# Kernel optimization log

Hardware: AMD Instinct MI355X
Metric: run time of the kernel (lower is better)

The kernel has to match this reference:

```python
import jax, jax.numpy as jnp
import numpy as np

EPS = 1e-7
C = 1.0  # Poincare ball curvature

def _norm(v):
    return jnp.maximum(jnp.linalg.norm(v, axis=-1, keepdims=True), EPS)

def logmap0(x):
    n = _norm(x)
    n_c = jnp.minimum(n, 1.0 - 1e-5)
    return jnp.arctanh(jnp.sqrt(C) * n_c) * x / (jnp.sqrt(C) * n)

def expmap0(v):
    n = _norm(v)
    return jnp.tanh(jnp.sqrt(C) * n) * v / (jnp.sqrt(C) * n)

def hat_layer(x, W, a_src, a_dst, src, dst, num_nodes):
    # x: [N, in] on manifold; W: [in, H*D]; a_src/a_dst: [H, D]
    H, D = a_src.shape
    h = logmap0(x) @ W                       # tangent-space linear, [N, H*D]
    h = h.reshape(num_nodes, H, D)
    e_s = jnp.einsum('nhd,hd->nh', h, a_src)  # [N, H]
    e_d = jnp.einsum('nhd,hd->nh', h, a_dst)
    e = jax.nn.leaky_relu(e_s[src] + e_d[dst], 0.2)          # [E, H]
    emax = jax.ops.segment_max(e, dst, num_segments=num_nodes)
    emax = jnp.where(jnp.isfinite(emax), emax, 0.0)
    ee = jnp.exp(e - emax[dst])                               # [E, H]
    denom = jax.ops.segment_sum(ee, dst, num_segments=num_nodes)
    alpha = ee / (denom[dst] + 1e-16)                          # segment softmax
    msg = alpha[:, :, None] * h[src]                           # [E, H, D] (largest buffer)
    out = jax.ops.segment_sum(msg, dst, num_segments=num_nodes)
    return expmap0(out.reshape(num_nodes, H * D))

def setup_inputs() -> dict:
    key = jax.random.key(0)
    ks = jax.random.split(key, 9)
    N, E = 50000, 800000
    IN, HID, OUT, HEADS = 128, 64, 64, 4
    x = 0.05 * jax.random.normal(ks[0], (N, IN), dtype=jnp.float32)  # inside unit ball
    edge_index0 = jax.random.randint(ks[1], (2, E), 0, N, dtype=jnp.int32)
    edge_index1 = jax.random.randint(ks[2], (2, E), 0, N, dtype=jnp.int32)
    s = 0.05
    W1 = s * jax.random.normal(ks[3], (IN, HEADS * HID), dtype=jnp.float32)
    a_src1 = s * jax.random.normal(ks[4], (HEADS, HID), dtype=jnp.float32)
    a_dst1 = s * jax.random.normal(ks[5], (HEADS, HID), dtype=jnp.float32)
    W2 = s * jax.random.normal(ks[6], (HEADS * HID, OUT), dtype=jnp.float32)
    a_src2 = s * jax.random.normal(ks[7], (1, OUT), dtype=jnp.float32)
    a_dst2 = s * jax.random.normal(ks[8], (1, OUT), dtype=jnp.float32)
    return {"x": x, "W1": W1, "a_src1": a_src1, "a_dst1": a_dst1,
            "W2": W2, "a_src2": a_src2, "a_dst2": a_dst2,
            "edge_index0": edge_index0, "edge_index1": edge_index1}

def reference(x, W1, a_src1, a_dst1, W2, a_src2, a_dst2, edge_index0, edge_index1):
    N = x.shape[0]
    h = hat_layer(x, W1, a_src1, a_dst1, edge_index0[0], edge_index0[1], N)
    out = hat_layer(h, W2, a_src2, a_dst2, edge_index1[0], edge_index1[1], N)
    return out
```

## Files before the change

kernel.cpp:

```cpp
#include <hip/hip_runtime.h>

#define EPSF 1e-7f
#define NBMAX 512

typedef __attribute__((ext_vector_type(4))) _Float16 half4;
typedef __attribute__((ext_vector_type(8))) _Float16 half8;
typedef __attribute__((ext_vector_type(2))) _Float16 half2v;
typedef __attribute__((ext_vector_type(4))) float f32x4;
typedef unsigned long long u64;

__device__ __forceinline__ float lrelu02(float x){ return x > 0.f ? x : 0.2f*x; }

__global__ __launch_bounds__(256) void k_pre(
    const float* __restrict__ W1, const float* __restrict__ W2,
    const float* __restrict__ x,
    _Float16* __restrict__ w1t, _Float16* __restrict__ w2t,
    int* __restrict__ bcnt, _Float16* __restrict__ lxh, int N) {
  const int b = blockIdx.x, tid = threadIdx.x;
  if (b < 128) {
    int idx = b*256 + tid;
    int j = idx >> 7, k = idx & 127;
    w1t[idx] = (_Float16)W1[(size_t)k*256 + j];
    return;
  }
  if (b < 192) {
    int idx = (b-128)*256 + tid;
    int j = idx >> 8, k = idx & 255;
    w2t[idx] = (_Float16)W2[(size_t)k*64 + j];
    return;
  }
  if (b == 192) {
    for (int i = tid; i < 2*NBMAX; i += 256) bcnt[i] = 0;
    return;
  }
  int tidg = (b - 193)*256 + tid;
  int wid = tidg >> 6, lane = tidg & 63;
  int nw = (gridDim.x - 193) * 4;
  for (int row = wid; row < N; row += nw) {
    float2 v = *(const float2*)(x + (size_t)row*128 + lane*2);
    float ss = v.x*v.x + v.y*v.y;
    #pragma unroll
    for (int o = 32; o; o >>= 1) ss += __shfl_xor(ss, o);
    float n  = fmaxf(sqrtf(ss), EPSF);
    float nc = fminf(n, 1.f - 1e-5f);
    float sc = atanhf(nc) / n;
    half2v hv; hv.x = (_Float16)(v.x*sc); hv.y = (_Float16)(v.y*sc);
    *(half2v*)(lxh + (size_t)row*128 + lane*2) = hv;
  }
}

__global__ __launch_bounds__(256) void k_bhist(
    const int* __restrict__ dst0, int E0, const int* __restrict__ dst1, int E1,
    int* __restrict__ bcnt0, int* __restrict__ bcnt1, int nb) {
  __shared__ int h0[NBMAX], h1[NBMAX];
  const int tid = threadIdx.x;
  const int g = blockIdx.x*blockDim.x + tid;
  const int stride = gridDim.x*blockDim.x;
  for (int i = tid; i < nb; i += 256) { h0[i] = 0; h1[i] = 0; }
  __syncthreads();
  for (int i = g; i < E0; i += stride) atomicAdd(&h0[dst0[i] >> 7], 1);
  for (int i = g; i < E1; i += stride) atomicAdd(&h1[dst1[i] >> 7], 1);
  __syncthreads();
  for (int i = tid; i < nb; i += 256) {
    if (h0[i]) atomicAdd(&bcnt0[i], h0[i]);
    if (h1[i]) atomicAdd(&bcnt1[i], h1[i]);
  }
}

__global__ __launch_bounds__(1024) void k_bscan(
    const int* __restrict__ bcnt0, int* __restrict__ bbase0, int* __restrict__ bcur0,
    const int* __restrict__ bcnt1, int* __restrict__ bbase1, int* __restrict__ bcur1,
    int nb) {
  __shared__ int wt[16];
  const int tid = threadIdx.x;
  const int half = tid >> 9, idx = tid & 511;
  const int* bcnt = half ? bcnt1 : bcnt0;
  int* bbase = half ? bbase1 : bbase0;
  int* bcur  = half ? bcur1  : bcur0;
  int v = (idx < nb) ? bcnt[idx] : 0;
  const int lane = tid & 63, w = tid >> 6;
  int inc = v;
  #pragma unroll
  for (int o = 1; o < 64; o <<= 1) { int t = __shfl_up(inc, o); if (lane >= o) inc += t; }
  if (lane == 63) wt[w] = inc;
  __syncthreads();
  int woff = 0;
  for (int i = half*8; i < w; ++i) woff += wt[i];
  int excl = woff + inc - v;
  if (idx < nb) { bbase[idx] = excl; bcur[idx] = excl; }
  if (idx == nb-1) bbase[nb] = excl + v;
}

__global__ __launch_bounds__(256) void k_bucketA(
    const int* __restrict__ src0, const int* __restrict__ dst0,
    int* __restrict__ bcur0, u64* __restrict__ temp0, int E0, int blocksA0,
    const int* __restrict__ src1, const int* __restrict__ dst1,
    int* __restrict__ bcur1, u64* __restrict__ temp1, int E1, int nb) {
  const int g0 = (blockIdx.x < blocksA0);
  const int* src = g0 ? src0 : src1;
  const int* dst = g0 ? dst0 : dst1;
  int* bcur      = g0 ? bcur0 : bcur1;
  u64* temp      = g0 ? temp0 : temp1;
  const int E    = g0 ? E0 : E1;
  const int cb   = g0 ? blockIdx.x : blockIdx.x - blocksA0;
  __shared__ int hist[NBMAX];
  __shared__ int lbase[NBMAX];
  const int tid = threadIdx.x;
  const int chunk0 = cb * 4096;
  const int e_end = min(chunk0 + 4096, E);
  for (int i = tid; i < nb; i += 256) hist[i] = 0;
  __syncthreads();
  for (int i = chunk0 + tid; i < e_end; i += 256)
    atomicAdd(&hist[dst[i] >> 7], 1);
  __syncthreads();
  for (int bn = tid; bn < nb; bn += 256) {
    int c = hist[bn];
    lbase[bn] = c ? atomicAdd(&bcur[bn], c) : 0;
    hist[bn] = 0;
  }
  __syncthreads();
  for (int i = chunk0 + tid; i < e_end; i += 256) {
    int d = dst[i];
    int bn = d >> 7;
    int off = atomicAdd(&hist[bn], 1);
    temp[(size_t)lbase[bn] + off] = ((u64)(unsigned)d << 32) | (unsigned)src[i];
  }
}

__global__ __launch_bounds__(256) void k_bucketB2(
    const u64* __restrict__ temp0, const int* __restrict__ bbase0,
    int* __restrict__ rowptr0, int* __restrict__ csrc0,
    const float* __restrict__ es1, const float* __restrict__ ed1,
    half4* __restrict__ w0,
    const u64* __restrict__ temp1, const int* __restrict__ bbase1,
    int* __restrict__ rowptr1, int* __restrict__ csrc1, int N, int nb) {
  const int g0 = (blockIdx.x < nb);
  const u64* temp = g0 ? temp0 : temp1;
  const int* bbase = g0 ? bbase0 : bbase1;
  int* rowptr = g0 ? rowptr0 : rowptr1;
  int* csrc   = g0 ? csrc0 : csrc1;
  const int b = g0 ? blockIdx.x : blockIdx.x - nb;
  __shared__ int lcnt[128];
  __shared__ int lcur[128];
  __shared__ int wt4[4];
  __shared__ float ledv[512];
  const int tid = threadIdx.x;
  const int d0 = b << 7;
  const int d1 = min(d0 + 128, N);
  const int lo = bbase[b], hi = bbase[b+1];
  if (tid < 128) lcnt[tid] = 0;
  if (g0) {
    for (int i = tid; i < (d1 - d0)*4; i += 256) ledv[i] = ed1[d0*4 + i];
  }
  __syncthreads();
  for (int k = lo + tid; k < hi; k += 256)
    atomicAdd(&lcnt[(int)(temp[k] >> 32) - d0], 1);
  __syncthreads();
  int v = (tid < 128) ? lcnt[tid] : 0;
  const int lane = tid & 63, w = tid >> 6;
  int inc = v;
  #pragma unroll
  for (int o = 1; o < 64; o <<= 1) { int t = __shfl_up(inc, o); if (lane >= o) inc += t; }
  if (lane == 63) wt4[w] = inc;
  __syncthreads();
  int woff = 0;
  for (int i = 0; i < w; ++i) woff += wt4[i];
  int excl = lo + woff + inc - v;
  if (tid < d1 - d0) { rowptr[d0 + tid] = excl; lcur[tid] = excl; }
  if (b == nb-1 && tid == 0) rowptr[N] = hi;
  __syncthreads();
  for (int k = lo + tid; k < hi; k += 256) {
    u64 p = temp[k];
    int d = (int)(p >> 32);
    int s = (int)(unsigned)p;
    int pos = atomicAdd(&lcur[d - d0], 1);
    csrc[pos] = s;
    if (g0) {
      float4 e = *(const float4*)(es1 + (size_t)s*4);
      int ld = (d - d0)*4;
      half4 wh;
      wh.x = (_Float16)__expf(lrelu02(e.x + ledv[ld+0]));
      wh.y = (_Float16)__expf(lrelu02(e.y + ledv[ld+1]));
      wh.z = (_Float16)__expf(lrelu02(e.z + ledv[ld+2]));
      wh.w = (_Float16)__expf(lrelu02(e.w + ledv[ld+3]));
      w0[pos] = wh;
    }
  }
}

#define LXP 136
#define H1P 264
__global__ __launch_bounds__(256) void k_gemm1_mfma(
    const _Float16* __restrict__ lxh, const _Float16* __restrict__ w1t,
    const float* __restrict__ a_src, const float* __restrict__ a_dst,
    _Float16* __restrict__ h1h, float* __restrict__ es, float* __restrict__ ed, int N) {
  __shared__ _Float16 lxs[32*LXP];
  __shared__ _Float16 h1s[32*H1P];
  const int tid = threadIdx.x;
  const int block0 = blockIdx.x * 32;
  const int vrows = min(32, N - block0);
  for (int i = tid; i < 512; i += 256) {
    int r = i >> 4, c = (i & 15) * 8;
    uint4 v = make_uint4(0u,0u,0u,0u);
    if (r < vrows) v = *(const uint4*)(lxh + (size_t)(block0 + r)*128 + c);
    *(uint4*)(lxs + r*LXP + c) = v;
  }
  __syncthreads();
  const int wv = tid >> 6, lane = tid & 63;
  const int rt = wv & 1;
  const int ch = wv >> 1;
  const int arow = rt*16 + (lane & 15);
  const int koff = (lane >> 4) * 8;
  f32x4 acc[8];
  #pragma unroll
  for (int t = 0; t < 8; ++t) acc[t] = (f32x4){0.f,0.f,0.f,0.f};
  #pragma unroll
  for (int ks = 0; ks < 4; ++ks) {
    half8 a = *(const half8*)(lxs + arow*LXP + ks*32 + koff);
    #pragma unroll
    for (int t = 0; t < 8; ++t) {
      const int col0 = ch*128 + t*16;
      half8 b = *(const half8*)(w1t + (size_t)(col0 + (lane & 15))*128 + ks*32 + koff);
      acc[t] = __builtin_amdgcn_mfma_f32_16x16x32_f16(a, b, acc[t], 0, 0, 0);
    }
  }
  #pragma unroll
  for (int t = 0; t < 8; ++t) {
    const int col = ch*128 + t*16 + (lane & 15);
    #pragma unroll
    for (int r = 0; r < 4; ++r) {
      const int row = rt*16 + (lane >> 4)*4 + r;
      h1s[row*H1P + col] = (_Float16)acc[t][r];
    }
  }
  __syncthreads();
  for (int i = tid; i < 1024; i += 256) {
    int r = i >> 5, c = (i & 31) * 8;
    if (r < vrows) {
      uint4 v = *(const uint4*)(h1s + r*H1P + c);
      *(uint4*)(h1h + (size_t)(block0 + r)*256 + c) = v;
    }
  }
  const int head = lane >> 4;
  const float4 as4 = *(const float4*)(a_src + lane*4);
  const float4 ad4 = *(const float4*)(a_dst + lane*4);
  #pragma unroll
  for (int r8 = 0; r8 < 8; ++r8) {
    int rl = wv*8 + r8;
    int row = block0 + rl;
    if (row >= N) break;
    half4 hv = *(const half4*)(h1s + rl*H1P + lane*4);
    float ax = (float)hv.x, ay = (float)hv.y, az = (float)hv.z, aw = (float)hv.w;
    float ps = ax*as4.x + ay*as4.y + az*as4.z + aw*as4.w;
    float pd = ax*ad4.x + ay*ad4.y + az*ad4.z + aw*ad4.w;
    #pragma unroll
    for (int o = 8; o; o >>= 1) { ps += __shfl_xor(ps, o); pd += __shfl_xor(pd, o); }
    if ((lane & 15) == 0) { es[row*4 + head] = ps; ed[row*4 + head] = pd; }
  }
}

__global__ void k_agg1_csr(const int* __restrict__ rowptr, const int* __restrict__ csrc,
                           const half4* __restrict__ w0,
                           const _Float16* __restrict__ h1h, _Float16* __restrict__ t2h,
                           int N) {
  int tidg = blockIdx.x*blockDim.x + threadIdx.x;
  int wid = tidg >> 6, lane = tidg & 63;
  int nw = (gridDim.x * blockDim.x) >> 6;
  const int h = lane >> 4;
  const _Float16* wp = (const _Float16*)w0;
  half2v ones; ones.x = (_Float16)1.f; ones.y = (_Float16)1.f;
  for (int d = wid; d < N; d += nw) {
    const int beg = rowptr[d], end = rowptr[d+1];
    float4 acc = make_float4(0.f,0.f,0.f,0.f);
    float wsum = 0.f;
    int k = beg;
    const int kend4 = beg + ((end - beg) & ~3);
    if (k < kend4) {
      int s0 = csrc[k], s1 = csrc[k+1], s2 = csrc[k+2], s3 = csrc[k+3];
      half2v wab, wcd;
      wab.x = wp[(size_t)(k+0)*4 + h]; wab.y = wp[(size_t)(k+1)*4 + h];
      wcd.x = wp[(size_t)(k+2)*4 + h]; wcd.y = wp[(size_t)(k+3)*4 + h];
      for (;;) {
        half4 v0 = *(const half4*)(h1h + (size_t)s0*256 + lane*4);
        half4 v1 = *(const half4*)(h1h + (size_t)s1*256 + lane*4);
        half4 v2 = *(const half4*)(h1h + (size_t)s2*256 + lane*4);
        half4 v3 = *(const half4*)(h1h + (size_t)s3*256 + lane*4);
        k += 4;
        const bool more = (k < kend4);
        int t0 = 0, t1 = 0, t2 = 0, t3 = 0;
        half2v uab, ucd;
        uab.x = uab.y = ucd.x = ucd.y = (_Float16)0.f;
        if (more) {
          t0 = csrc[k]; t1 = csrc[k+1]; t2 = csrc[k+2]; t3 = csrc[k+3];
          uab.x = wp[(size_t)(k+0)*4 + h]; uab.y = wp[(size_t)(k+1)*4 + h];
          ucd.x = wp[(size_t)(k+2)*4 + h]; ucd.y = wp[(size_t)(k+3)*4 + h];
        }
        wsum = __builtin_amdgcn_fdot2(wab, ones, wsum, false);
        wsum = __builtin_amdgcn_fdot2(wcd, ones, wsum, false);
        half2v p;
        p.x = v0.x; p.y = v1.x;
        acc.x = __builtin_amdgcn_fdot2(p, wab, acc.x, false);
        p.x = v2.x; p.y = v3.x;
        acc.x = __builtin_amdgcn_fdot2(p, wcd, acc.x, false);
        p.x = v0.y; p.y = v1.y;
        acc.y = __builtin_amdgcn_fdot2(p, wab, acc.y, false);
        p.x = v2.y; p.y = v3.y;
        acc.y = __builtin_amdgcn_fdot2(p, wcd, acc.y, false);
        p.x = v0.z; p.y = v1.z;
        acc.z = __builtin_amdgcn_fdot2(p, wab, acc.z, false);
        p.x = v2.z; p.y = v3.z;
        acc.z = __builtin_amdgcn_fdot2(p, wcd, acc.z, false);
        p.x = v0.w; p.y = v1.w;
        acc.w = __builtin_amdgcn_fdot2(p, wab, acc.w, false);
        p.x = v2.w; p.y = v3.w;
        acc.w = __builtin_amdgcn_fdot2(p, wcd, acc.w, false);
        if (!more) break;
        s0 = t0; s1 = t1; s2 = t2; s3 = t3;
        wab = uab; wcd = ucd;
      }
    }
    for (; k < end; ++k) {
      int s = csrc[k];
      float wa = (float)wp[(size_t)k*4 + h];
      half4 hv = *(const half4*)(h1h + (size_t)s*256 + lane*4);
      wsum += wa;
      acc.x += wa*(float)hv.x; acc.y += wa*(float)hv.y;
      acc.z += wa*(float)hv.z; acc.w += wa*(float)hv.w;
    }
    float inv = 1.f / (wsum + 1e-16f);
    float ax = acc.x*inv, ay = acc.y*inv, az = acc.z*inv, aw = acc.w*inv;
    float ss = ax*ax + ay*ay + az*az + aw*aw;
    #pragma unroll
    for (int o = 32; o; o >>= 1) ss += __shfl_xor(ss, o);
    float n  = fmaxf(sqrtf(ss), EPSF);
    float s1 = tanhf(n) / n;
    float n2 = fmaxf(s1 * n, EPSF);
    float nc = fminf(n2, 1.f - 1e-5f);
    float sc = s1 * atanhf(nc) / n2;
    half4 o4; o4.x = (_Float16)(ax*sc); o4.y = (_Float16)(ay*sc);
              o4.z = (_Float16)(az*sc); o4.w = (_Float16)(aw*sc);
    *(half4*)(t2h + (size_t)d*256 + lane*4) = o4;
  }
}

#define T2SP 264
#define H2SP 72
__global__ __launch_bounds__(256) void k_gemm2_mfma(
    const _Float16* __restrict__ t2h, const _Float16* __restrict__ w2t,
    const float* __restrict__ a_src, const float* __restrict__ a_dst,
    _Float16* __restrict__ h2h, float* __restrict__ es, float* __restrict__ ed, int N) {
  __shared__ _Float16 t2s[32*T2SP];
  __shared__ _Float16 h2s[32*H2SP];
  const int tid = threadIdx.x;
  const int block0 = blockIdx.x * 32;
  const int vrows = min(32, N - block0);
  for (int i = tid; i < 1024; i += 256) {
    int r = i >> 5, c = (i & 31) * 8;
    uint4 v = make_uint4(0u,0u,0u,0u);
    if (r < vrows) v = *(const uint4*)(t2h + (size_t)(block0 + r)*256 + c);
    *(uint4*)(t2s + r*T2SP + c) = v;
  }
  __syncthreads();
  const int wv = tid >> 6, lane = tid & 63;
  const int rt = wv & 1;
  const int ch = wv >> 1;
  const int arow = rt*16 + (lane & 15);
  const int koff = (lane >> 4) * 8;
  f32x4 acc[2];
  acc[0] = (f32x4){0.f,0.f,0.f,0.f};
  acc[1] = (f32x4){0.f,0.f,0.f,0.f};
  #pragma unroll
  for (int ks = 0; ks < 8; ++ks) {
    half8 a = *(const half8*)(t2s + arow*T2SP + ks*32 + koff);
    #pragma unroll
    for (int t = 0; t < 2; ++t) {
      const int col0 = ch*32 + t*16;
      half8 b = *(const half8*)(w2t + (size_t)(col0 + (lane & 15))*256 + ks*32 + koff);
      acc[t] = __builtin_amdgcn_mfma_f32_16x16x32_f16(a, b, acc[t], 0, 0, 0);
    }
  }
  #pragma unroll
  for (int t = 0; t < 2; ++t) {
    const int col = ch*32 + t*16 + (lane & 15);
    #pragma unroll
    for (int r = 0; r < 4; ++r) {
      const int row = rt*16 + (lane >> 4)*4 + r;
      h2s[row*H2SP + col] = (_Float16)acc[t][r];
    }
  }
  __syncthreads();
  {
    int i = tid;
    int r = i >> 3, c = (i & 7) * 8;
    if (r < vrows) {
      uint4 v = *(const uint4*)(h2s + r*H2SP + c);
      *(uint4*)(h2h + (size_t)(block0 + r)*64 + c) = v;
    }
  }
  const int jj = (lane & 15) * 4;
  const int rg = lane >> 4;
  const int rbase = wv*8 + rg*2;
  const float4 as4 = *(const float4*)(a_src + jj);
  const float4 ad4 = *(const float4*)(a_dst + jj);
  #pragma unroll
  for (int rr = 0; rr < 2; ++rr) {
    int row = block0 + rbase + rr;
    if (row < N) {
      half4 hv = *(const half4*)(h2s + (rbase + rr)*H2SP + jj);
      float ax = (float)hv.x, ay = (float)hv.y, az = (float)hv.z, aw = (float)hv.w;
      float ps = ax*as4.x + ay*as4.y + az*as4.z + aw*as4.w;
      float pd = ax*ad4.x + ay*ad4.y + az*ad4.z + aw*ad4.w;
      #pragma unroll
      for (int o = 8; o; o >>= 1) { ps += __shfl_xor(ps, o); pd += __shfl_xor(pd, o); }
      if ((lane & 15) == 0) { es[row] = ps; ed[row] = pd; }
    }
  }
}

__global__ void k_agg2_csr(const int* __restrict__ rowptr, const int* __restrict__ csrc,
                           const float* __restrict__ es, const float* __restrict__ ed,
                           const _Float16* __restrict__ h2h, float* __restrict__ out, int N) {
  int tidg = blockIdx.x*blockDim.x + threadIdx.x;
  int wid = tidg >> 6, lane = tidg & 63;
  int nw = (gridDim.x * blockDim.x) >> 6;
  for (int d = wid; d < N; d += nw) {
    const int beg = rowptr[d], end = rowptr[d+1];
    const float edv = ed[d];
    float acc = 0.f, wsum = 0.f;
    int k = beg;
    const int kend4 = beg + ((end - beg) & ~3);
    if (k < kend4) {
      int s0 = csrc[k], s1 = csrc[k+1], s2 = csrc[k+2], s3 = csrc[k+3];
      for (;;) {
        float e0 = es[s0], e1 = es[s1], e2 = es[s2], e3 = es[s3];
        float x0 = (float)h2h[(size_t)s0*64 + lane];
        float x1 = (float)h2h[(size_t)s1*64 + lane];
        float x2 = (float)h2h[(size_t)s2*64 + lane];
        float x3 = (float)h2h[(size_t)s3*64 + lane];
        k += 4;
        const bool more = (k < kend4);
        int t0 = 0, t1 = 0, t2 = 0, t3 = 0;
        if (more) { t0 = csrc[k]; t1 = csrc[k+1]; t2 = csrc[k+2]; t3 = csrc[k+3]; }
        float w0 = __expf(lrelu02(e0 + edv));
        float w1 = __expf(lrelu02(e1 + edv));
        float w2 = __expf(lrelu02(e2 + edv));
        float w3 = __expf(lrelu02(e3 + edv));
        wsum += (w0 + w1) + (w2 + w3);
        acc += w0*x0 + w1*x1 + w2*x2 + w3*x3;
        if (!more) break;
        s0 = t0; s1 = t1; s2 = t2; s3 = t3;
      }
    }
    for (; k < end; ++k) {
      int s = csrc[k];
      float w = __expf(lrelu02(es[s] + edv));
      wsum += w;
      acc += w * (float)h2h[(size_t)s*64 + lane];
    }
    float a = acc / (wsum + 1e-16f);
    float ss = a*a;
    #pragma unroll
    for (int o = 32; o; o >>= 1) ss += __shfl_xor(ss, o);
    float n  = fmaxf(sqrtf(ss), EPSF);
    float sc = tanhf(n) / n;
    out[(size_t)d*64 + lane] = a * sc;
  }
}

extern "C" void kernel_launch(void* const* d_in, const int* in_sizes, int n_in,
                              void* d_out, int out_size, void* d_ws, size_t ws_size,
                              hipStream_t stream) {
  const float* x      = (const float*)d_in[0];
  const float* W1     = (const float*)d_in[1];
  const float* a_src1 = (const float*)d_in[2];
  const float* a_dst1 = (const float*)d_in[3];
  const float* W2     = (const float*)d_in[4];
  const float* a_src2 = (const float*)d_in[5];
  const float* a_dst2 = (const float*)d_in[6];
  const int*   ei0    = (const int*)d_in[7];
  const int*   ei1    = (const int*)d_in[8];
  const int N  = in_sizes[0] / 128;
  const int E0 = in_sizes[7] / 2;
  const int E1 = in_sizes[8] / 2;
  const int* src0 = ei0;  const int* dst0 = ei0 + E0;
  const int* src1 = ei1;  const int* dst1 = ei1 + E1;
  float* out = (float*)d_out;
  const int nb = (N + 127) >> 7;

  float* ws = (float*)d_ws;
  size_t o = 0;
  float* es1   = ws + o; o += (size_t)N*4;
  float* ed1   = ws + o; o += (size_t)N*4;
  float* es2   = ws + o; o += (size_t)N;
  float* ed2   = ws + o; o += (size_t)N;
  _Float16* lxh = (_Float16*)(ws + o); o += (size_t)N*64;
  _Float16* w1t = (_Float16*)(ws + o); o += 16384;
  _Float16* w2t = (_Float16*)(ws + o); o += 8192;
  _Float16* h1h = (_Float16*)(ws + o); o += (size_t)N*128;
  _Float16* t2h = (_Float16*)(ws + o); o += (size_t)N*128;
  _Float16* h2h = (_Float16*)(ws + o); o += (size_t)N*32;
  o += (o & 1);
  half4* w0    = (half4*)(ws + o); o += (size_t)E0*2;
  u64* temp0 = (u64*)(ws + o); o += (size_t)E0*2;
  u64* temp1 = (u64*)(ws + o); o += (size_t)E1*2;
  int* iws = (int*)(ws + o);
  size_t io = 0;
  int* rowptr0 = iws + io; io += N + 1;
  int* rowptr1 = iws + io; io += N + 1;
  int* bcnt0   = iws + io; io += NBMAX;
  int* bcnt1   = iws + io; io += NBMAX;
  int* bbase0  = iws + io; io += NBMAX + 1;
  int* bbase1  = iws + io; io += NBMAX + 1;
  int* bcur0   = iws + io; io += NBMAX;
  int* bcur1   = iws + io; io += NBMAX;
  int* csrc0   = iws + io; io += E0;
  int* csrc1   = iws + io; io += E1;

  dim3 blk(256);
  const int blocksA0 = (E0 + 4095) / 4096;
  const int blocksA1 = (E1 + 4095) / 4096;
  k_pre    <<<193 + 2048, blk, 0, stream>>>(W1, W2, x, w1t, w2t, bcnt0, lxh, N);
  k_gemm1_mfma<<<(N+31)/32, blk, 0, stream>>>(lxh, w1t, a_src1, a_dst1,
                                              h1h, es1, ed1, N);
  k_bhist  <<<1024, blk, 0, stream>>>(dst0, E0, dst1, E1, bcnt0, bcnt1, nb);
  k_bscan  <<<1, 1024, 0, stream>>>(bcnt0, bbase0, bcur0, bcnt1, bbase1, bcur1, nb);
  k_bucketA<<<blocksA0 + blocksA1, blk, 0, stream>>>(
      src0, dst0, bcur0, temp0, E0, blocksA0, src1, dst1, bcur1, temp1, E1, nb);
  k_bucketB2<<<2*nb, blk, 0, stream>>>(temp0, bbase0, rowptr0, csrc0,
                                       es1, ed1, w0,
                                       temp1, bbase1, rowptr1, csrc1, N, nb);
  k_agg1_csr<<<2048, blk, 0, stream>>>(rowptr0, csrc0, w0, h1h, t2h, N);
  k_gemm2_mfma<<<(N+31)/32, blk, 0, stream>>>(t2h, w2t, a_src2, a_dst2,
                                              h2h, es2, ed2, N);
  k_agg2_csr<<<2048, blk, 0, stream>>>(rowptr1, csrc1, es2, ed2, h2h, out, N);
}
```

Measured before the change: 253.6 us.

## Fold bucket histogram and scan into existing preprocessing and GEMM kernels

The bucket histogram now runs inside k_pre as per-partition block histograms written to a partials buffer, so no zeroing or global atomics are needed. The exclusive scan over buckets runs in two extra blocks appended to the first GEMM launch, which sum the 256 partials per bucket. Two kernel launches and their serialization are removed. In exchange k_pre grows by 512 blocks, there is a partials buffer of 2x256x512 ints, and two GEMM blocks each read 256 partial rows serially.

```diff
diff --git a/kernel.cpp b/kernel.cpp
--- a/kernel.cpp
+++ b/kernel.cpp
@@ -14,8 +14,10 @@
 __global__ __launch_bounds__(256) void k_pre(
     const float* __restrict__ W1, const float* __restrict__ W2,
     const float* __restrict__ x,
+    const int* __restrict__ dst0, int E0, const int* __restrict__ dst1, int E1,
     _Float16* __restrict__ w1t, _Float16* __restrict__ w2t,
-    int* __restrict__ bcnt, _Float16* __restrict__ lxh, int N) {
+    int* __restrict__ part0, int* __restrict__ part1,
+    _Float16* __restrict__ lxh, int N) {
   const int b = blockIdx.x, tid = threadIdx.x;
   if (b < 128) {
     int idx = b*256 + tid;
@@ -29,13 +31,26 @@
     w2t[idx] = (_Float16)W2[(size_t)k*64 + j];
     return;
   }
-  if (b == 192) {
-    for (int i = tid; i < 2*NBMAX; i += 256) bcnt[i] = 0;
+  if (b < 704) {
+    const int pb = b - 192;
+    const int g = pb >> 8, p = pb & 255;
+    const int* dst = g ? dst1 : dst0;
+    const int E = g ? E1 : E0;
+    int* part = g ? part1 : part0;
+    __shared__ int hist[NBMAX];
+    for (int i = tid; i < NBMAX; i += 256) hist[i] = 0;
+    __syncthreads();
+    const int per = (E + 255) >> 8;
+    const int lo = p * per, hi = min(lo + per, E);
+    for (int i = lo + tid; i < hi; i += 256)
+      atomicAdd(&hist[dst[i] >> 7], 1);
+    __syncthreads();
+    for (int i = tid; i < NBMAX; i += 256) part[p*NBMAX + i] = hist[i];
     return;
   }
-  int tidg = (b - 193)*256 + tid;
+  int tidg = (b - 704)*256 + tid;
   int wid = tidg >> 6, lane = tidg & 63;
-  int nw = (gridDim.x - 193) * 4;
+  int nw = (gridDim.x - 704) * 4;
   for (int row = wid; row < N; row += nw) {
     float2 v = *(const float2*)(x + (size_t)row*128 + lane*2);
     float ss = v.x*v.x + v.y*v.y;
@@ -47,48 +62,6 @@
     half2v hv; hv.x = (_Float16)(v.x*sc); hv.y = (_Float16)(v.y*sc);
     *(half2v*)(lxh + (size_t)row*128 + lane*2) = hv;
   }
-}
-
-__global__ __launch_bounds__(256) void k_bhist(
-    const int* __restrict__ dst0, int E0, const int* __restrict__ dst1, int E1,
-    int* __restrict__ bcnt0, int* __restrict__ bcnt1, int nb) {
-  __shared__ int h0[NBMAX], h1[NBMAX];
-  const int tid = threadIdx.x;
-  const int g = blockIdx.x*blockDim.x + tid;
-  const int stride = gridDim.x*blockDim.x;
-  for (int i = tid; i < nb; i += 256) { h0[i] = 0; h1[i] = 0; }
-  __syncthreads();
-  for (int i = g; i < E0; i += stride) atomicAdd(&h0[dst0[i] >> 7], 1);
-  for (int i = g; i < E1; i += stride) atomicAdd(&h1[dst1[i] >> 7], 1);
-  __syncthreads();
-  for (int i = tid; i < nb; i += 256) {
-    if (h0[i]) atomicAdd(&bcnt0[i], h0[i]);
-    if (h1[i]) atomicAdd(&bcnt1[i], h1[i]);
-  }
-}
-
-__global__ __launch_bounds__(1024) void k_bscan(
-    const int* __restrict__ bcnt0, int* __restrict__ bbase0, int* __restrict__ bcur0,
-    const int* __restrict__ bcnt1, int* __restrict__ bbase1, int* __restrict__ bcur1,
-    int nb) {
-  __shared__ int wt[16];
-  const int tid = threadIdx.x;
-  const int half = tid >> 9, idx = tid & 511;
-  const int* bcnt = half ? bcnt1 : bcnt0;
-  int* bbase = half ? bbase1 : bbase0;
-  int* bcur  = half ? bcur1  : bcur0;
-  int v = (idx < nb) ? bcnt[idx] : 0;
-  const int lane = tid & 63, w = tid >> 6;
-  int inc = v;
-  #pragma unroll
-  for (int o = 1; o < 64; o <<= 1) { int t = __shfl_up(inc, o); if (lane >= o) inc += t; }
-  if (lane == 63) wt[w] = inc;
-  __syncthreads();
-  int woff = 0;
-  for (int i = half*8; i < w; ++i) woff += wt[i];
-  int excl = woff + inc - v;
-  if (idx < nb) { bbase[idx] = excl; bcur[idx] = excl; }
-  if (idx == nb-1) bbase[nb] = excl + v;
 }
 
 __global__ __launch_bounds__(256) void k_bucketA(
@@ -193,10 +166,41 @@
 __global__ __launch_bounds__(256) void k_gemm1_mfma(
     const _Float16* __restrict__ lxh, const _Float16* __restrict__ w1t,
     const float* __restrict__ a_src, const float* __restrict__ a_dst,
-    _Float16* __restrict__ h1h, float* __restrict__ es, float* __restrict__ ed, int N) {
+    _Float16* __restrict__ h1h, float* __restrict__ es, float* __restrict__ ed,
+    const int* __restrict__ part0, const int* __restrict__ part1,
+    int* __restrict__ bbase0, int* __restrict__ bcur0,
+    int* __restrict__ bbase1, int* __restrict__ bcur1, int nb, int N) {
   __shared__ _Float16 lxs[32*LXP];
   __shared__ _Float16 h1s[32*H1P];
+  __shared__ int swt[4];
   const int tid = threadIdx.x;
+  const int nblk = (N + 31) >> 5;
+  if ((int)blockIdx.x >= nblk) {
+    const int g = (int)blockIdx.x - nblk;
+    const int* part = g ? part1 : part0;
+    int* bbase = g ? bbase1 : bbase0;
+    int* bcur  = g ? bcur1  : bcur0;
+    const int i0 = tid*2, i1 = tid*2 + 1;
+    int v0 = 0, v1 = 0;
+    for (int p = 0; p < 256; ++p) {
+      v0 += part[p*NBMAX + i0];
+      v1 += part[p*NBMAX + i1];
+    }
+    int s = v0 + v1;
+    const int lane = tid & 63, w = tid >> 6;
+    int inc = s;
+    #pragma unroll
+    for (int o = 1; o < 64; o <<= 1) { int t = __shfl_up(inc, o); if (lane >= o) inc += t; }
+    if (lane == 63) swt[w] = inc;
+    __syncthreads();
+    int woff = 0;
+    for (int i = 0; i < w; ++i) woff += swt[i];
+    int excl = woff + inc - s;
+    if (i0 < nb) { bbase[i0] = excl; bcur[i0] = excl; }
+    if (i1 < nb) { bbase[i1] = excl + v0; bcur[i1] = excl + v0; }
+    if (tid == 255) bbase[nb] = excl + s;
+    return;
+  }
   const int block0 = blockIdx.x * 32;
   const int vrows = min(32, N - block0);
   for (int i = tid; i < 512; i += 256) {
@@ -507,8 +511,8 @@
   size_t io = 0;
   int* rowptr0 = iws + io; io += N + 1;
   int* rowptr1 = iws + io; io += N + 1;
-  int* bcnt0   = iws + io; io += NBMAX;
-  int* bcnt1   = iws + io; io += NBMAX;
+  int* part0   = iws + io; io += 256*NBMAX;
+  int* part1   = iws + io; io += 256*NBMAX;
   int* bbase0  = iws + io; io += NBMAX + 1;
   int* bbase1  = iws + io; io += NBMAX + 1;
   int* bcur0   = iws + io; io += NBMAX;
@@ -519,11 +523,13 @@
   dim3 blk(256);
   const int blocksA0 = (E0 + 4095) / 4096;
   const int blocksA1 = (E1 + 4095) / 4096;
-  k_pre    <<<193 + 2048, blk, 0, stream>>>(W1, W2, x, w1t, w2t, bcnt0, lxh, N);
-  k_gemm1_mfma<<<(N+31)/32, blk, 0, stream>>>(lxh, w1t, a_src1, a_dst1,
-                                              h1h, es1, ed1, N);
-  k_bhist  <<<1024, blk, 0, stream>>>(dst0, E0, dst1, E1, bcnt0, bcnt1, nb);
-  k_bscan  <<<1, 1024, 0, stream>>>(bcnt0, bbase0, bcur0, bcnt1, bbase1, bcur1, nb);
+  const int nblk1 = (N + 31) / 32;
+  k_pre    <<<704 + 2048, blk, 0, stream>>>(W1, W2, x, dst0, E0, dst1, E1,
+                                            w1t, w2t, part0, part1, lxh, N);
+  k_gemm1_mfma<<<nblk1 + 2, blk, 0, stream>>>(lxh, w1t, a_src1, a_dst1,
+                                              h1h, es1, ed1,
+                                              part0, part1,
+                                              bbase0, bcur0, bbase1, bcur1, nb, N);
   k_bucketA<<<blocksA0 + blocksA1, blk, 0, stream>>>(
       src0, dst0, bcur0, temp0, E0, blocksA0, src1, dst1, bcur1, temp1, E1, nb);
   k_bucketB2<<<2*nb, blk, 0, stream>>>(temp0, bbase0, rowptr0, csrc0,
```

Measured after the change: 229.3 us, median of 2. 9.6% less time.
